# Optimization experiments

Hardware: AMD Instinct MI355X
Metric: run time of the kernel (lower is better)

The kernel has to match this reference:

```python
import jax, jax.numpy as jnp
import numpy as np

N, D = 131072, 512
G, NG = 512, 256  # G groups of equal size NG, contiguous; N == G*NG
MARGIN, LAMBDA_CD, LAMBDA_CDD, LAMBDA_PCC, K_MARGIN = 2.0, 0.0, 1.0, 1.0, 0.02
EPS = 1e-6


def setup_inputs() -> dict:
    key = jax.random.key(0)
    k1, k2, k3, k4 = jax.random.split(key, 4)
    z_r = jax.random.normal(k1, (N, D), jnp.float32)
    z_r = z_r / jnp.linalg.norm(z_r, axis=-1, keepdims=True)
    z_v = jax.random.normal(k2, (N, D), jnp.float32)
    z_v = z_v / jnp.linalg.norm(z_v, axis=-1, keepdims=True)
    labels = jax.random.randint(k3, (N,), 0, 2)
    groups = jnp.repeat(jnp.arange(G), NG)  # contiguous equal-size groups
    var_lens = jax.random.randint(k4, (N,), 0, 10000)
    return {"z_r": z_r, "z_v": z_v, "labels": labels, "groups": groups, "var_lens": var_lens}


def reference(z_r, z_v, labels, groups, var_lens):
    # cosine distance per pair: [N]
    d = 1.0 - jnp.sum(z_r * z_v, axis=-1)

    mb = (labels == 0).astype(d.dtype)
    mp = (labels == 1).astype(d.dtype)
    nb, npos = mb.sum(), mp.sum()
    db_mean = jnp.sum(d * mb) / jnp.maximum(nb, 1.0)
    dp_mean = jnp.sum(d * mp) / jnp.maximum(npos, 1.0)

    l_cd = jnp.where(nb > 0, db_mean, 0.0)
    l_cdd = jnp.where((nb > 0) & (npos > 0),
                      jax.nn.relu(MARGIN + db_mean - dp_mean), 0.0)

    # --- per-group losses, vectorized over G equal-size contiguous groups ---
    d_g = d.reshape(G, NG)                                   # [G, n_g]
    v_g = var_lens.reshape(G, NG).astype(d.dtype)            # [G, n_g]

    # Pearson-style z-score matching loss (torch std is unbiased, ddof=1)
    v_std = jnp.std(v_g, axis=1, ddof=1)
    d_std = jnp.std(d_g, axis=1, ddof=1)
    v_z = (v_g - v_g.mean(axis=1, keepdims=True)) / (v_std + EPS)[:, None]
    d_z = (d_g - d_g.mean(axis=1, keepdims=True)) / (d_std + EPS)[:, None]
    corr_loss = jnp.mean((v_z - d_z) ** 2, axis=1)
    corr_loss = jnp.where((v_std > 0) & (d_std > 0), corr_loss, 0.0)

    # sort each group by var_len
    order = jnp.argsort(v_g, axis=1)
    v_s = jnp.take_along_axis(v_g, order, axis=1)            # [G, n_g]
    d_s = jnp.take_along_axis(d_g, order, axis=1)            # [G, n_g]

    # neighbor monotonicity violation
    neigh_viol = jnp.mean(jax.nn.relu(d_s[:, :-1] - d_s[:, 1:] + K_MARGIN), axis=1)

    # pairwise rank loss: dv[g,i,j] = v_s[g,j] - v_s[g,i] (matches torch unsqueeze(0)-unsqueeze(1))
    dv = v_s[:, None, :] - v_s[:, :, None]                   # [G, n_g, n_g]
    dd = d_s[:, None, :] - d_s[:, :, None]                   # [G, n_g, n_g]
    mask = (dv > 0).astype(d.dtype)
    cnt = mask.sum(axis=(1, 2))
    pair_sum = jnp.sum(jax.nn.relu(K_MARGIN - dd) * mask, axis=(1, 2))
    rank_loss = jnp.where(cnt > 0, pair_sum / jnp.maximum(cnt, 1.0), 0.0)

    group_loss = corr_loss + neigh_viol + rank_loss          # [G]
    # size-weighted sum; all groups have equal size NG -> plain mean
    l_pcc = jnp.mean(group_loss)

    total = LAMBDA_CD * l_cd + LAMBDA_CDD * l_cdd + LAMBDA_PCC * l_pcc
    return total, l_cdd, l_pcc, d
```

## Files before the change

kernel.cpp:

```cpp
#include <hip/hip_runtime.h>

#define NTOT   131072
#define DIMV   512
#define GCNT   512
#define NGRP   256
#define KMARG  0.02f
#define CMARG  2.0f
#define EPSC   1e-6f

typedef float f4 __attribute__((ext_vector_type(4)));

template <int NW, int M>
__device__ __forceinline__ void block_sum_m(float* v, float* red) {
  const int t = threadIdx.x;
#pragma unroll
  for (int m = 0; m < M; ++m) {
#pragma unroll
    for (int off = 32; off; off >>= 1) v[m] += __shfl_down(v[m], off, 64);
  }
  __syncthreads();
  if ((t & 63) == 0) {
#pragma unroll
    for (int m = 0; m < M; ++m) red[(t >> 6) * M + m] = v[m];
  }
  __syncthreads();
#pragma unroll
  for (int m = 0; m < M; ++m) {
    float s = 0.0f;
#pragma unroll
    for (int i = 0; i < NW; ++i) s += red[i * M + m];
    v[m] = s;
  }
}

__device__ __forceinline__ float wave_sum(float v) {
#pragma unroll
  for (int off = 32; off; off >>= 1) v += __shfl_down(v, off, 64);
  return v;
}

__global__ __launch_bounds__(256) void dot_kernel(const float* __restrict__ zr,
                                                  const float* __restrict__ zv,
                                                  float* __restrict__ dout) {
  const int wave = threadIdx.x >> 6;
  const int lane = threadIdx.x & 63;
  const int row0 = ((blockIdx.x << 2) + wave) << 1;
  const f4* r = (const f4*)zr + ((size_t)row0 << 7);
  const f4* v = (const f4*)zv + ((size_t)row0 << 7);
  f4 a0 = __builtin_nontemporal_load(r + lane);
  f4 b0 = __builtin_nontemporal_load(v + lane);
  f4 a1 = __builtin_nontemporal_load(r + lane + 64);
  f4 b1 = __builtin_nontemporal_load(v + lane + 64);
  f4 a2 = __builtin_nontemporal_load(r + lane + 128);
  f4 b2 = __builtin_nontemporal_load(v + lane + 128);
  f4 a3 = __builtin_nontemporal_load(r + lane + 192);
  f4 b3 = __builtin_nontemporal_load(v + lane + 192);
  f4 p = a0 * b0 + a1 * b1;
  f4 q = a2 * b2 + a3 * b3;
  float s0 = wave_sum(p.x + p.y + p.z + p.w);
  float s1 = wave_sum(q.x + q.y + q.z + q.w);
  if (lane == 0) {
    dout[row0]     = 1.0f - s0;
    dout[row0 + 1] = 1.0f - s1;
  }
}

__global__ __launch_bounds__(256) void group_kernel(const float* __restrict__ d,
                                                    const int* __restrict__ labels,
                                                    const int* __restrict__ varl,
                                                    float* __restrict__ gout) {
  __shared__ float  red[4 * 4];
  __shared__ float2 skv[NGRP];
  __shared__ float  sdat[NGRP];
  const int g = blockIdx.x, t = threadIdx.x;
  const int idx = g * NGRP + t;
  const float dv  = d[idx];
  const float vv  = (float)varl[idx];
  const int   lab = labels[idx];

  skv[t] = make_float2(vv, dv);

  float sA[4] = {dv, vv, (lab == 0) ? dv : 0.0f, (lab == 0) ? 1.0f : 0.0f};
  block_sum_m<4, 4>(sA, red);
  const float sumd = sA[0], sumv = sA[1], sb = sA[2], cb = sA[3];
  const float md = sumd * (1.0f / NGRP), mv = sumv * (1.0f / NGRP);

  const float vdev = vv - mv, ddev = dv - md;
  float sB[3] = {vdev * vdev, ddev * ddev, vdev * ddev};
  block_sum_m<4, 3>(sB, red);
  const float svv = sB[0], sdd = sB[1], svd = sB[2];
  const float vstd = sqrtf(svv * (1.0f / (NGRP - 1)));
  const float dstd = sqrtf(sdd * (1.0f / (NGRP - 1)));
  const float iv = 1.0f / (vstd + EPSC), id = 1.0f / (dstd + EPSC);
  float corr = (svv * iv * iv + sdd * id * id - 2.0f * svd * iv * id) * (1.0f / NGRP);
  corr = (vstd > 0.0f && dstd > 0.0f) ? corr : 0.0f;

  __syncthreads();
  int rank = 0;
  float pc = 0.0f, ps = 0.0f;
  const float pre = KMARG + dv;
  for (int j = 0; j < NGRP; ++j) {
    const float2 kv = skv[j];
    const float vj = kv.x, dj = kv.y;
    if (vj > vv) {
      pc += 1.0f;
      ps += fmaxf(pre - dj, 0.0f);
    }
    rank += (vj < vv || (vj == vv && j < t)) ? 1 : 0;
  }
  sdat[rank] = dv;
  __syncthreads();
  const float nv = (t < NGRP - 1) ? fmaxf(sdat[t] - sdat[t + 1] + KMARG, 0.0f) : 0.0f;

  float sC[3] = {ps, pc, nv};
  block_sum_m<4, 3>(sC, red);
  const float rank_loss = (sC[1] > 0.0f) ? sC[0] / fmaxf(sC[1], 1.0f) : 0.0f;
  const float neigh = sC[2] * (1.0f / (NGRP - 1));

  if (t == 0) {
    gout[g]            = corr + neigh + rank_loss;
    gout[GCNT + g]     = sb;
    gout[2 * GCNT + g] = cb;
    gout[3 * GCNT + g] = sumd;
  }
}

__global__ __launch_bounds__(512) void final_kernel(const float* __restrict__ gout,
                                                    float* __restrict__ out) {
  __shared__ float red[8 * 4];
  const int t = threadIdx.x;
  float s[4] = {gout[t], gout[GCNT + t], gout[2 * GCNT + t], gout[3 * GCNT + t]};
  block_sum_m<8, 4>(s, red);
  if (t == 0) {
    const float L = s[0], SB = s[1], CB = s[2], SumD = s[3];
    const float SP = SumD - SB;
    const float CP = (float)NTOT - CB;
    const float db = SB / fmaxf(CB, 1.0f);
    const float dp = SP / fmaxf(CP, 1.0f);
    const float l_cdd = (CB > 0.0f && CP > 0.0f) ? fmaxf(CMARG + db - dp, 0.0f) : 0.0f;
    const float l_pcc = L * (1.0f / GCNT);
    out[0] = l_cdd + l_pcc;
    out[1] = l_cdd;
    out[2] = l_pcc;
  }
}

extern "C" void kernel_launch(void* const* d_in, const int* in_sizes, int n_in,
                              void* d_out, int out_size, void* d_ws, size_t ws_size,
                              hipStream_t stream) {
  const float* zr     = (const float*)d_in[0];
  const float* zv     = (const float*)d_in[1];
  const int*   labels = (const int*)d_in[2];
  const int*   varl   = (const int*)d_in[4];
  float* out  = (float*)d_out;
  float* dvec = out + 3;
  float* gws  = (float*)d_ws;

  dot_kernel<<<NTOT / 8, 256, 0, stream>>>(zr, zv, dvec);
  group_kernel<<<GCNT, 256, 0, stream>>>(dvec, labels, varl, gws);
  final_kernel<<<1, 512, 0, stream>>>(gws, out);
}
```

Before: 114.5 us.

## Fuse row dot-product kernel into per-group loss kernel

Merges the cosine-distance streaming kernel into the per-group loss kernel. Each of the 512 blocks now computes the 256 distances of its own group, keeps them in shared memory, and still writes them to the output vector. This removes one kernel launch and the global re-read of the distance vector. In exchange, the 512 MB streaming load is spread over only 512 blocks instead of 16384, which may lower memory-level parallelism and occupancy on a bandwidth-bound pass.

Result: no change. 113.8 us (-0.6%).

```diff
diff --git a/kernel.cpp b/kernel.cpp
--- a/kernel.cpp
+++ b/kernel.cpp
@@ -39,42 +39,50 @@
   return v;
 }
 
-__global__ __launch_bounds__(256) void dot_kernel(const float* __restrict__ zr,
-                                                  const float* __restrict__ zv,
-                                                  float* __restrict__ dout) {
-  const int wave = threadIdx.x >> 6;
-  const int lane = threadIdx.x & 63;
-  const int row0 = ((blockIdx.x << 2) + wave) << 1;
-  const f4* r = (const f4*)zr + ((size_t)row0 << 7);
-  const f4* v = (const f4*)zv + ((size_t)row0 << 7);
-  f4 a0 = __builtin_nontemporal_load(r + lane);
-  f4 b0 = __builtin_nontemporal_load(v + lane);
-  f4 a1 = __builtin_nontemporal_load(r + lane + 64);
-  f4 b1 = __builtin_nontemporal_load(v + lane + 64);
-  f4 a2 = __builtin_nontemporal_load(r + lane + 128);
-  f4 b2 = __builtin_nontemporal_load(v + lane + 128);
-  f4 a3 = __builtin_nontemporal_load(r + lane + 192);
-  f4 b3 = __builtin_nontemporal_load(v + lane + 192);
-  f4 p = a0 * b0 + a1 * b1;
-  f4 q = a2 * b2 + a3 * b3;
-  float s0 = wave_sum(p.x + p.y + p.z + p.w);
-  float s1 = wave_sum(q.x + q.y + q.z + q.w);
-  if (lane == 0) {
-    dout[row0]     = 1.0f - s0;
-    dout[row0 + 1] = 1.0f - s1;
-  }
-}
-
-__global__ __launch_bounds__(256) void group_kernel(const float* __restrict__ d,
+__global__ __launch_bounds__(256) void fused_kernel(const float* __restrict__ zr,
+                                                    const float* __restrict__ zv,
                                                     const int* __restrict__ labels,
                                                     const int* __restrict__ varl,
+                                                    float* __restrict__ dvec,
                                                     float* __restrict__ gout) {
   __shared__ float  red[4 * 4];
+  __shared__ float  sd[NGRP];
   __shared__ float2 skv[NGRP];
   __shared__ float  sdat[NGRP];
   const int g = blockIdx.x, t = threadIdx.x;
+  const int wave = t >> 6, lane = t & 63;
+
+  const size_t rowbase = (size_t)g * NGRP;
+#pragma unroll 2
+  for (int it = 0; it < NGRP / 8; ++it) {
+    const int rg = it * 8 + wave * 2;
+    const size_t row0 = rowbase + rg;
+    const f4* r = (const f4*)zr + (row0 << 7);
+    const f4* v = (const f4*)zv + (row0 << 7);
+    f4 a0 = __builtin_nontemporal_load(r + lane);
+    f4 b0 = __builtin_nontemporal_load(v + lane);
+    f4 a1 = __builtin_nontemporal_load(r + lane + 64);
+    f4 b1 = __builtin_nontemporal_load(v + lane + 64);
+    f4 a2 = __builtin_nontemporal_load(r + lane + 128);
+    f4 b2 = __builtin_nontemporal_load(v + lane + 128);
+    f4 a3 = __builtin_nontemporal_load(r + lane + 192);
+    f4 b3 = __builtin_nontemporal_load(v + lane + 192);
+    f4 p = a0 * b0 + a1 * b1;
+    f4 q = a2 * b2 + a3 * b3;
+    float s0 = wave_sum(p.x + p.y + p.z + p.w);
+    float s1 = wave_sum(q.x + q.y + q.z + q.w);
+    if (lane == 0) {
+      const float d0 = 1.0f - s0, d1 = 1.0f - s1;
+      sd[rg]     = d0;
+      sd[rg + 1] = d1;
+      dvec[row0]     = d0;
+      dvec[row0 + 1] = d1;
+    }
+  }
+  __syncthreads();
+
   const int idx = g * NGRP + t;
-  const float dv  = d[idx];
+  const float dv  = sd[t];
   const float vv  = (float)varl[idx];
   const int   lab = labels[idx];
 
@@ -95,7 +103,6 @@
   float corr = (svv * iv * iv + sdd * id * id - 2.0f * svd * iv * id) * (1.0f / NGRP);
   corr = (vstd > 0.0f && dstd > 0.0f) ? corr : 0.0f;
 
-  __syncthreads();
   int rank = 0;
   float pc = 0.0f, ps = 0.0f;
   const float pre = KMARG + dv;
@@ -156,7 +163,6 @@
   float* dvec = out + 3;
   float* gws  = (float*)d_ws;
 
-  dot_kernel<<<NTOT / 8, 256, 0, stream>>>(zr, zv, dvec);
-  group_kernel<<<GCNT, 256, 0, stream>>>(dvec, labels, varl, gws);
+  fused_kernel<<<GCNT, 256, 0, stream>>>(zr, zv, labels, varl, dvec, gws);
   final_kernel<<<1, 512, 0, stream>>>(gws, out);
 }
```
